# Optimization experiments

Measured on AMD Instinct MI355X. Metric: run time of the kernel, lower is better.

Reference implementation:

```python
import jax, jax.numpy as jnp
import numpy as np

B, L, C, H = 4, 1024, 768, 12
D = C // H  # head_ch = 64


def setup_inputs() -> dict:
    key = jax.random.key(0)
    ks = jax.random.split(key, 8)
    s = 1.0 / np.sqrt(C)
    return {
        "inputs_q": jax.random.normal(ks[0], (B, L, C), jnp.float32),
        "inputs_kv": jax.random.normal(ks[1], (B, L, C), jnp.float32),
        "Wq": jax.random.normal(ks[2], (C, H * D), jnp.float32) * s,
        "Wk": jax.random.normal(ks[3], (C, H * D), jnp.float32) * s,
        "Wv": jax.random.normal(ks[4], (C, H * D), jnp.float32) * s,
        "Wout": jax.random.normal(ks[5], (H * D, C), jnp.float32) * s,
        "W_pre": jax.random.normal(ks[6], (H, H), jnp.float32) * (1.0 / np.sqrt(H)),
        "W_post": jax.random.normal(ks[7], (H, H), jnp.float32) * (1.0 / np.sqrt(H)),
    }


def reference(inputs_q, inputs_kv, Wq, Wk, Wv, Wout, W_pre, W_post):
    # Linear projections (no bias), split into heads: b l (h d) -> b h l d
    def split_heads(x):
        b, l, _ = x.shape
        return x.reshape(b, l, H, D).transpose(0, 2, 1, 3)

    q = split_heads(inputs_q @ Wq) / jnp.sqrt(jnp.asarray(D, inputs_q.dtype))
    k = split_heads(inputs_kv @ Wk)
    v = split_heads(inputs_kv @ Wv)

    # Attention logits [b, h, l, k]
    weights = jnp.einsum('bhld,bhkd->bhlk', q, k)
    # Talking-heads: learned cross-head mixing pre-softmax
    weights = jnp.einsum('bhlk,hi->bilk', weights, W_pre)
    weights = jax.nn.softmax(weights, axis=-1)
    # Talking-heads post-softmax mixing
    weights = jnp.einsum('bhlk,hi->bilk', weights, W_post)

    scores = jnp.einsum('bhlk,bhkd->bhld', weights, v)
    scores = scores.transpose(0, 2, 1, 3).reshape(B, L, H * D)  # b l (h d)
    return scores @ Wout
```

## Files before the change

kernel.cpp:

```cpp
#include <hip/hip_runtime.h>

#define BB 4
#define LL 1024
#define CC 768
#define HH 12
#define DD 64

typedef unsigned short ushort_t;
typedef __attribute__((ext_vector_type(8))) short bf16x8;
typedef __attribute__((ext_vector_type(4))) float f32x4;

__device__ inline ushort_t f2bf(float x) {
    union { float f; unsigned u; } v; v.f = x;
    unsigned r = (v.u + 0x7FFFu + ((v.u >> 16) & 1u)) >> 16;
    return (ushort_t)r;
}
__device__ inline float bf2f(ushort_t u) {
    union { unsigned u; float f; } v; v.u = ((unsigned)u) << 16;
    return v.f;
}

__global__ __launch_bounds__(256) void cast_in(const float* __restrict__ q,
                                               const float* __restrict__ kv,
                                               ushort_t* __restrict__ qo,
                                               ushort_t* __restrict__ kvo) {
    const float* src = blockIdx.y ? kv : q;
    ushort_t* dst = blockIdx.y ? kvo : qo;
    size_t i = ((size_t)blockIdx.x * 256 + threadIdx.x) * 8;
    float4 a = *(const float4*)(src + i);
    float4 b = *(const float4*)(src + i + 4);
    ushort_t t[8] = {f2bf(a.x), f2bf(a.y), f2bf(a.z), f2bf(a.w),
                     f2bf(b.x), f2bf(b.y), f2bf(b.z), f2bf(b.w)};
    *(uint4*)(dst + i) = *(uint4*)t;
}

__global__ __launch_bounds__(256) void wt_cast(const float* __restrict__ w0, const float* __restrict__ w1,
                                               const float* __restrict__ w2, const float* __restrict__ w3,
                                               ushort_t* __restrict__ o0, ushort_t* __restrict__ o1,
                                               ushort_t* __restrict__ o2, ushort_t* __restrict__ o3) {
    const float* W = blockIdx.z == 0 ? w0 : blockIdx.z == 1 ? w1 : blockIdx.z == 2 ? w2 : w3;
    ushort_t* Wt   = blockIdx.z == 0 ? o0 : blockIdx.z == 1 ? o1 : blockIdx.z == 2 ? o2 : o3;
    __shared__ float t[32][33];
    const int c = threadIdx.x & 31, r0 = threadIdx.x >> 5;
    const int kb = blockIdx.x * 32, nb = blockIdx.y * 32;
#pragma unroll
    for (int i = 0; i < 4; ++i)
        t[r0 + 8 * i][c] = W[(size_t)(kb + r0 + 8 * i) * CC + nb + c];
    __syncthreads();
#pragma unroll
    for (int i = 0; i < 4; ++i)
        Wt[(size_t)(nb + r0 + 8 * i) * CC + kb + c] = f2bf(t[c][r0 + 8 * i]);
}

__global__ __launch_bounds__(256) void proj_gemm(const ushort_t* __restrict__ Aq,
                                                 const ushort_t* __restrict__ Akv,
                                                 const ushort_t* __restrict__ Wqt,
                                                 const ushort_t* __restrict__ Wkt,
                                                 const ushort_t* __restrict__ Wvt,
                                                 ushort_t* __restrict__ Qo,
                                                 ushort_t* __restrict__ Ko,
                                                 ushort_t* __restrict__ Vto) {
    const int z = blockIdx.z;
    const ushort_t* A  = (z == 0) ? Aq : Akv;
    const ushort_t* Wt = (z == 0) ? Wqt : (z == 1 ? Wkt : Wvt);

    __shared__ ushort_t a_lds[128 * 40];
    __shared__ ushort_t b_lds[128 * 40];

    const int tid = threadIdx.x;
    const int bm = blockIdx.x * 128, bn = blockIdx.y * 128;
    const int wave = tid >> 6, lane = tid & 63;
    const int quad = lane >> 4, lq = lane & 15;
    const int wr = wave >> 1, wc = wave & 1;

    f32x4 acc[4][4] = {};

    for (int k0 = 0; k0 < CC; k0 += 32) {
#pragma unroll
        for (int s = 0; s < 2; ++s) {
            int c = tid + s * 256;
            int row = c >> 2, ko = (c & 3) * 8;
            *(uint4*)&a_lds[row * 40 + ko] = *(const uint4*)&A[(size_t)(bm + row) * CC + k0 + ko];
            *(uint4*)&b_lds[row * 40 + ko] = *(const uint4*)&Wt[(size_t)(bn + row) * CC + k0 + ko];
        }
        __syncthreads();
        bf16x8 af[4], bfr[4];
#pragma unroll
        for (int mi = 0; mi < 4; ++mi)
            af[mi] = *(bf16x8*)&a_lds[(wr * 64 + mi * 16 + lq) * 40 + quad * 8];
#pragma unroll
        for (int ni = 0; ni < 4; ++ni)
            bfr[ni] = *(bf16x8*)&b_lds[(wc * 64 + ni * 16 + lq) * 40 + quad * 8];
#pragma unroll
        for (int mi = 0; mi < 4; ++mi)
#pragma unroll
            for (int ni = 0; ni < 4; ++ni)
                acc[mi][ni] = __builtin_amdgcn_mfma_f32_16x16x32_bf16(af[mi], bfr[ni], acc[mi][ni], 0, 0, 0);
        __syncthreads();
    }

    const float scale = (z == 0) ? 0.125f : 1.0f;
#pragma unroll
    for (int mi = 0; mi < 4; ++mi)
#pragma unroll
        for (int ni = 0; ni < 4; ++ni)
#pragma unroll
            for (int r = 0; r < 4; ++r) {
                int row = bm + wr * 64 + mi * 16 + quad * 4 + r;
                int col = bn + wc * 64 + ni * 16 + lq;
                int b = row >> 10, l = row & 1023, h = col >> 6, d = col & 63;
                ushort_t v = f2bf(acc[mi][ni][r] * scale);
                if (z == 0)      Qo[((size_t)(b * HH + h) * LL + l) * DD + d] = v;
                else if (z == 1) Ko[((size_t)(b * HH + h) * LL + l) * DD + d] = v;
                else             Vto[((size_t)(b * HH + h) * DD + d) * LL + l] = v;
            }
}

__global__ __launch_bounds__(256) void qk_gemm(const ushort_t* __restrict__ Q,
                                               const ushort_t* __restrict__ K,
                                               ushort_t* __restrict__ S) {
    __shared__ ushort_t a_lds[128 * 40];
    __shared__ ushort_t b_lds[128 * 40];

    const int tid = threadIdx.x;
    const int bm = blockIdx.x * 128, bn = blockIdx.y * 128;
    const int bh = blockIdx.z;
    const ushort_t* Qh = Q + (size_t)bh * LL * DD;
    const ushort_t* Kh = K + (size_t)bh * LL * DD;
    const int wave = tid >> 6, lane = tid & 63;
    const int quad = lane >> 4, lq = lane & 15;
    const int wr = wave >> 1, wc = wave & 1;

    f32x4 acc[4][4] = {};

    for (int k0 = 0; k0 < DD; k0 += 32) {
#pragma unroll
        for (int s = 0; s < 2; ++s) {
            int c = tid + s * 256;
            int row = c >> 2, ko = (c & 3) * 8;
            *(uint4*)&a_lds[row * 40 + ko] = *(const uint4*)&Qh[(size_t)(bm + row) * DD + k0 + ko];
            *(uint4*)&b_lds[row * 40 + ko] = *(const uint4*)&Kh[(size_t)(bn + row) * DD + k0 + ko];
        }
        __syncthreads();
        bf16x8 af[4], bfr[4];
#pragma unroll
        for (int mi = 0; mi < 4; ++mi)
            af[mi] = *(bf16x8*)&a_lds[(wr * 64 + mi * 16 + lq) * 40 + quad * 8];
#pragma unroll
        for (int ni = 0; ni < 4; ++ni)
            bfr[ni] = *(bf16x8*)&b_lds[(wc * 64 + ni * 16 + lq) * 40 + quad * 8];
#pragma unroll
        for (int mi = 0; mi < 4; ++mi)
#pragma unroll
            for (int ni = 0; ni < 4; ++ni)
                acc[mi][ni] = __builtin_amdgcn_mfma_f32_16x16x32_bf16(af[mi], bfr[ni], acc[mi][ni], 0, 0, 0);
        __syncthreads();
    }

#pragma unroll
    for (int mi = 0; mi < 4; ++mi)
#pragma unroll
        for (int ni = 0; ni < 4; ++ni)
#pragma unroll
            for (int r = 0; r < 4; ++r) {
                int row = bm + wr * 64 + mi * 16 + quad * 4 + r;
                int col = bn + wc * 64 + ni * 16 + lq;
                S[((size_t)bh * LL + row) * LL + col] = f2bf(acc[mi][ni][r]);
            }
}

__global__ __launch_bounds__(256) void mix_softmax(ushort_t* __restrict__ S,
                                                   const float* __restrict__ Wpre,
                                                   const float* __restrict__ Wpost) {
    __shared__ float s[HH][LL];
    __shared__ float wpre[HH][HH];
    __shared__ float wpost[HH][HH];

    const int tid = threadIdx.x;
    const int l = blockIdx.x;
    const int b = blockIdx.y;

    if (tid < HH * HH) {
        wpre[tid / HH][tid % HH] = Wpre[tid];
        wpost[tid / HH][tid % HH] = Wpost[tid];
    }

    for (int idx = tid; idx < HH * 128; idx += 256) {
        int h = idx >> 7, c = idx & 127;
        uint4 raw = *(const uint4*)&S[((size_t)(b * HH + h) * LL + l) * LL + c * 8];
        ushort_t* u = (ushort_t*)&raw;
#pragma unroll
        for (int j = 0; j < 8; ++j) s[h][c * 8 + j] = bf2f(u[j]);
    }
    __syncthreads();

    for (int k = tid; k < LL; k += 256) {
        float sv[HH], mx[HH];
#pragma unroll
        for (int h = 0; h < HH; ++h) sv[h] = s[h][k];
#pragma unroll
        for (int i = 0; i < HH; ++i) {
            float a = 0.f;
#pragma unroll
            for (int h = 0; h < HH; ++h) a += sv[h] * wpre[h][i];
            mx[i] = a;
        }
#pragma unroll
        for (int i = 0; i < HH; ++i) s[i][k] = mx[i];
    }
    __syncthreads();

    {
        const int wave = tid >> 6;
        const int lane = tid & 63;
        for (int h = wave; h < HH; h += 4) {
            float vals[16];
            float m = -1e30f;
#pragma unroll
            for (int j = 0; j < 16; ++j) {
                vals[j] = s[h][lane + 64 * j];
                m = fmaxf(m, vals[j]);
            }
#pragma unroll
            for (int off = 32; off; off >>= 1) m = fmaxf(m, __shfl_xor(m, off));
            float sum = 0.f;
#pragma unroll
            for (int j = 0; j < 16; ++j) {
                vals[j] = __expf(vals[j] - m);
                sum += vals[j];
            }
#pragma unroll
            for (int off = 32; off; off >>= 1) sum += __shfl_xor(sum, off);
            float inv = 1.0f / sum;
#pragma unroll
            for (int j = 0; j < 16; ++j) s[h][lane + 64 * j] = vals[j] * inv;
        }
    }
    __syncthreads();

    for (int k = tid; k < LL; k += 256) {
        float sv[HH], mx[HH];
#pragma unroll
        for (int h = 0; h < HH; ++h) sv[h] = s[h][k];
#pragma unroll
        for (int i = 0; i < HH; ++i) {
            float a = 0.f;
#pragma unroll
            for (int h = 0; h < HH; ++h) a += sv[h] * wpost[h][i];
            mx[i] = a;
        }
#pragma unroll
        for (int i = 0; i < HH; ++i) s[i][k] = mx[i];
    }
    __syncthreads();

    for (int idx = tid; idx < HH * 128; idx += 256) {
        int h = idx >> 7, c = idx & 127;
        ushort_t u[8];
#pragma unroll
        for (int j = 0; j < 8; ++j) u[j] = f2bf(s[h][c * 8 + j]);
        *(uint4*)&S[((size_t)(b * HH + h) * LL + l) * LL + c * 8] = *(uint4*)u;
    }
}

__global__ __launch_bounds__(256) void pv_gemm(const ushort_t* __restrict__ P,
                                               const ushort_t* __restrict__ Vt,
                                               ushort_t* __restrict__ att) {
    __shared__ ushort_t a_lds[128 * 40];
    __shared__ ushort_t b_lds[64 * 40];

    const int tid = threadIdx.x;
    const int bm = blockIdx.x * 128;
    const int bh = blockIdx.y;
    const int b = bh / HH, ih = bh % HH;
    const ushort_t* Ph = P + ((size_t)bh << 20);
    const ushort_t* Vh = Vt + (size_t)bh * LL * DD;
    const int wave = tid >> 6, lane = tid & 63;
    const int quad = lane >> 4, lq = lane & 15;
    const int wr = wave >> 1, wc = wave & 1;

    f32x4 acc[4][2] = {};

    for (int k0 = 0; k0 < LL; k0 += 32) {
#pragma unroll
        for (int s = 0; s < 2; ++s) {
            int c = tid + s * 256;
            int row = c >> 2, ko = (c & 3) * 8;
            *(uint4*)&a_lds[row * 40 + ko] = *(const uint4*)&Ph[(size_t)(bm + row) * LL + k0 + ko];
        }
        {
            int row = tid >> 2, ko = (tid & 3) * 8;
            *(uint4*)&b_lds[row * 40 + ko] = *(const uint4*)&Vh[(size_t)row * LL + k0 + ko];
        }
        __syncthreads();
        bf16x8 af[4], bfr[2];
#pragma unroll
        for (int mi = 0; mi < 4; ++mi)
            af[mi] = *(bf16x8*)&a_lds[(wr * 64 + mi * 16 + lq) * 40 + quad * 8];
#pragma unroll
        for (int ni = 0; ni < 2; ++ni)
            bfr[ni] = *(bf16x8*)&b_lds[(wc * 32 + ni * 16 + lq) * 40 + quad * 8];
#pragma unroll
        for (int mi = 0; mi < 4; ++mi)
#pragma unroll
            for (int ni = 0; ni < 2; ++ni)
                acc[mi][ni] = __builtin_amdgcn_mfma_f32_16x16x32_bf16(af[mi], bfr[ni], acc[mi][ni], 0, 0, 0);
        __syncthreads();
    }

#pragma unroll
    for (int mi = 0; mi < 4; ++mi)
#pragma unroll
        for (int ni = 0; ni < 2; ++ni)
#pragma unroll
            for (int r = 0; r < 4; ++r) {
                int lrow = bm + wr * 64 + mi * 16 + quad * 4 + r;
                int col = wc * 32 + ni * 16 + lq;
                att[((size_t)(b * LL) + lrow) * CC + ih * DD + col] = f2bf(acc[mi][ni][r]);
            }
}

__global__ __launch_bounds__(256) void out_gemm(const ushort_t* __restrict__ A,
                                                const ushort_t* __restrict__ Wt,
                                                float* __restrict__ out) {
    __shared__ ushort_t a_lds[128 * 40];
    __shared__ ushort_t b_lds[128 * 40];

    const int tid = threadIdx.x;
    const int bm = blockIdx.x * 128, bn = blockIdx.y * 128;
    const int wave = tid >> 6, lane = tid & 63;
    const int quad = lane >> 4, lq = lane & 15;
    const int wr = wave >> 1, wc = wave & 1;

    f32x4 acc[4][4] = {};

    for (int k0 = 0; k0 < CC; k0 += 32) {
#pragma unroll
        for (int s = 0; s < 2; ++s) {
            int c = tid + s * 256;
            int row = c >> 2, ko = (c & 3) * 8;
            *(uint4*)&a_lds[row * 40 + ko] = *(const uint4*)&A[(size_t)(bm + row) * CC + k0 + ko];
            *(uint4*)&b_lds[row * 40 + ko] = *(const uint4*)&Wt[(size_t)(bn + row) * CC + k0 + ko];
        }
        __syncthreads();
        bf16x8 af[4], bfr[4];
#pragma unroll
        for (int mi = 0; mi < 4; ++mi)
            af[mi] = *(bf16x8*)&a_lds[(wr * 64 + mi * 16 + lq) * 40 + quad * 8];
#pragma unroll
        for (int ni = 0; ni < 4; ++ni)
            bfr[ni] = *(bf16x8*)&b_lds[(wc * 64 + ni * 16 + lq) * 40 + quad * 8];
#pragma unroll
        for (int mi = 0; mi < 4; ++mi)
#pragma unroll
            for (int ni = 0; ni < 4; ++ni)
                acc[mi][ni] = __builtin_amdgcn_mfma_f32_16x16x32_bf16(af[mi], bfr[ni], acc[mi][ni], 0, 0, 0);
        __syncthreads();
    }

#pragma unroll
    for (int mi = 0; mi < 4; ++mi)
#pragma unroll
        for (int ni = 0; ni < 4; ++ni)
#pragma unroll
            for (int r = 0; r < 4; ++r) {
                int row = bm + wr * 64 + mi * 16 + quad * 4 + r;
                int col = bn + wc * 64 + ni * 16 + lq;
                out[(size_t)row * CC + col] = acc[mi][ni][r];
            }
}

extern "C" void kernel_launch(void* const* d_in, const int* in_sizes, int n_in,
                              void* d_out, int out_size, void* d_ws, size_t ws_size,
                              hipStream_t stream) {
    const float* inputs_q  = (const float*)d_in[0];
    const float* inputs_kv = (const float*)d_in[1];
    const float* Wq   = (const float*)d_in[2];
    const float* Wk   = (const float*)d_in[3];
    const float* Wv   = (const float*)d_in[4];
    const float* Wout = (const float*)d_in[5];
    const float* Wpre  = (const float*)d_in[6];
    const float* Wpost = (const float*)d_in[7];
    float* out = (float*)d_out;

    const size_t nS   = (size_t)BB * HH * LL * LL;
    const size_t nQKV = (size_t)BB * HH * LL * DD;
    const size_t nW   = (size_t)CC * CC;

    ushort_t* Sb   = (ushort_t*)d_ws;
    ushort_t* Qb   = Sb + nS;
    ushort_t* Kb   = Qb + nQKV;
    ushort_t* Vtb  = Kb + nQKV;
    ushort_t* attb = Vtb + nQKV;
    ushort_t* inq  = attb + nQKV;
    ushort_t* inkv = inq + nQKV;
    ushort_t* Wqt  = inkv + nQKV;
    ushort_t* Wkt  = Wqt + nW;
    ushort_t* Wvt  = Wkt + nW;
    ushort_t* Wot  = Wvt + nW;

    dim3 blk(256);

    cast_in<<<dim3(1536, 2), blk, 0, stream>>>(inputs_q, inputs_kv, inq, inkv);
    wt_cast<<<dim3(24, 24, 4), blk, 0, stream>>>(Wq, Wk, Wv, Wout, Wqt, Wkt, Wvt, Wot);
    proj_gemm<<<dim3(32, 6, 3), blk, 0, stream>>>(inq, inkv, Wqt, Wkt, Wvt, Qb, Kb, Vtb);
    qk_gemm<<<dim3(8, 8, BB * HH), blk, 0, stream>>>(Qb, Kb, Sb);
    mix_softmax<<<dim3(LL, BB), blk, 0, stream>>>(Sb, Wpre, Wpost);
    pv_gemm<<<dim3(8, BB * HH), blk, 0, stream>>>(Sb, Vtb, attb);
    out_gemm<<<dim3(32, 6), blk, 0, stream>>>(attb, Wot, out);
}
```

Measured before the change: 269.7 us.

## Stage GEMM tiles via global_load_lds, halve pv tile, vectorize softmax LDS staging

Replaces register-staged global-to-LDS tile copies in all four GEMM kernels with direct global_load_lds 16-byte transfers into unpadded 32-element-wide LDS rows. The pv_gemm tile shrinks from 128 to 64 rows, doubling its grid, and mix_softmax switches to 4-wide loads and float4 LDS writes. The aim is to cut VGPR traffic and instruction count on the load path and raise pv_gemm occupancy. Dropping the row padding may cause LDS bank conflicts on the fragment reads.

```diff
diff --git a/kernel.cpp b/kernel.cpp
--- a/kernel.cpp
+++ b/kernel.cpp
@@ -18,6 +18,19 @@
 __device__ inline float bf2f(ushort_t u) {
     union { unsigned u; float f; } v; v.u = ((unsigned)u) << 16;
     return v.f;
+}
+
+__device__ inline void stage_rows(const ushort_t* __restrict__ g, int stride,
+                                  ushort_t* lds, int nbytes, int wave, int lane) {
+    const int ko = (lane & 3) << 3;
+    const int rsub = lane >> 2;
+    for (int off = wave * 1024; off < nbytes; off += 4096) {
+        int row = (off >> 6) + rsub;
+        __builtin_amdgcn_global_load_lds(
+            (const __attribute__((address_space(1))) void*)(g + (size_t)row * stride + ko),
+            (__attribute__((address_space(3))) void*)(lds + (off >> 1)),
+            16, 0, 0);
+    }
 }
 
 __global__ __launch_bounds__(256) void cast_in(const float* __restrict__ q,
@@ -64,8 +77,8 @@
     const ushort_t* A  = (z == 0) ? Aq : Akv;
     const ushort_t* Wt = (z == 0) ? Wqt : (z == 1 ? Wkt : Wvt);
 
-    __shared__ ushort_t a_lds[128 * 40];
-    __shared__ ushort_t b_lds[128 * 40];
+    __shared__ __align__(16) ushort_t a_lds[128 * 32];
+    __shared__ __align__(16) ushort_t b_lds[128 * 32];
 
     const int tid = threadIdx.x;
     const int bm = blockIdx.x * 128, bn = blockIdx.y * 128;
@@ -76,21 +89,16 @@
     f32x4 acc[4][4] = {};
 
     for (int k0 = 0; k0 < CC; k0 += 32) {
-#pragma unroll
-        for (int s = 0; s < 2; ++s) {
-            int c = tid + s * 256;
-            int row = c >> 2, ko = (c & 3) * 8;
-            *(uint4*)&a_lds[row * 40 + ko] = *(const uint4*)&A[(size_t)(bm + row) * CC + k0 + ko];
-            *(uint4*)&b_lds[row * 40 + ko] = *(const uint4*)&Wt[(size_t)(bn + row) * CC + k0 + ko];
-        }
+        stage_rows(A + (size_t)bm * CC + k0, CC, a_lds, 8192, wave, lane);
+        stage_rows(Wt + (size_t)bn * CC + k0, CC, b_lds, 8192, wave, lane);
         __syncthreads();
         bf16x8 af[4], bfr[4];
 #pragma unroll
         for (int mi = 0; mi < 4; ++mi)
-            af[mi] = *(bf16x8*)&a_lds[(wr * 64 + mi * 16 + lq) * 40 + quad * 8];
-#pragma unroll
-        for (int ni = 0; ni < 4; ++ni)
-            bfr[ni] = *(bf16x8*)&b_lds[(wc * 64 + ni * 16 + lq) * 40 + quad * 8];
+            af[mi] = *(bf16x8*)&a_lds[(wr * 64 + mi * 16 + lq) * 32 + quad * 8];
+#pragma unroll
+        for (int ni = 0; ni < 4; ++ni)
+            bfr[ni] = *(bf16x8*)&b_lds[(wc * 64 + ni * 16 + lq) * 32 + quad * 8];
 #pragma unroll
         for (int mi = 0; mi < 4; ++mi)
 #pragma unroll
@@ -119,8 +127,8 @@
 __global__ __launch_bounds__(256) void qk_gemm(const ushort_t* __restrict__ Q,
                                                const ushort_t* __restrict__ K,
                                                ushort_t* __restrict__ S) {
-    __shared__ ushort_t a_lds[128 * 40];
-    __shared__ ushort_t b_lds[128 * 40];
+    __shared__ __align__(16) ushort_t a_lds[128 * 32];
+    __shared__ __align__(16) ushort_t b_lds[128 * 32];
 
     const int tid = threadIdx.x;
     const int bm = blockIdx.x * 128, bn = blockIdx.y * 128;
@@ -134,21 +142,16 @@
     f32x4 acc[4][4] = {};
 
     for (int k0 = 0; k0 < DD; k0 += 32) {
-#pragma unroll
-        for (int s = 0; s < 2; ++s) {
-            int c = tid + s * 256;
-            int row = c >> 2, ko = (c & 3) * 8;
-            *(uint4*)&a_lds[row * 40 + ko] = *(const uint4*)&Qh[(size_t)(bm + row) * DD + k0 + ko];
-            *(uint4*)&b_lds[row * 40 + ko] = *(const uint4*)&Kh[(size_t)(bn + row) * DD + k0 + ko];
-        }
+        stage_rows(Qh + (size_t)bm * DD + k0, DD, a_lds, 8192, wave, lane);
+        stage_rows(Kh + (size_t)bn * DD + k0, DD, b_lds, 8192, wave, lane);
         __syncthreads();
         bf16x8 af[4], bfr[4];
 #pragma unroll
         for (int mi = 0; mi < 4; ++mi)
-            af[mi] = *(bf16x8*)&a_lds[(wr * 64 + mi * 16 + lq) * 40 + quad * 8];
-#pragma unroll
-        for (int ni = 0; ni < 4; ++ni)
-            bfr[ni] = *(bf16x8*)&b_lds[(wc * 64 + ni * 16 + lq) * 40 + quad * 8];
+            af[mi] = *(bf16x8*)&a_lds[(wr * 64 + mi * 16 + lq) * 32 + quad * 8];
+#pragma unroll
+        for (int ni = 0; ni < 4; ++ni)
+            bfr[ni] = *(bf16x8*)&b_lds[(wc * 64 + ni * 16 + lq) * 32 + quad * 8];
 #pragma unroll
         for (int mi = 0; mi < 4; ++mi)
 #pragma unroll
@@ -185,12 +188,12 @@
         wpost[tid / HH][tid % HH] = Wpost[tid];
     }
 
-    for (int idx = tid; idx < HH * 128; idx += 256) {
-        int h = idx >> 7, c = idx & 127;
-        uint4 raw = *(const uint4*)&S[((size_t)(b * HH + h) * LL + l) * LL + c * 8];
+    for (int idx = tid; idx < HH * 256; idx += 256) {
+        int h = idx >> 8, c = idx & 255;
+        uint2 raw = *(const uint2*)&S[((size_t)(b * HH + h) * LL + l) * LL + c * 4];
         ushort_t* u = (ushort_t*)&raw;
-#pragma unroll
-        for (int j = 0; j < 8; ++j) s[h][c * 8 + j] = bf2f(u[j]);
+        float4 f = make_float4(bf2f(u[0]), bf2f(u[1]), bf2f(u[2]), bf2f(u[3]));
+        ((float4*)s[h])[c] = f;
     }
     __syncthreads();
 
@@ -254,23 +257,22 @@
     }
     __syncthreads();
 
-    for (int idx = tid; idx < HH * 128; idx += 256) {
-        int h = idx >> 7, c = idx & 127;
-        ushort_t u[8];
-#pragma unroll
-        for (int j = 0; j < 8; ++j) u[j] = f2bf(s[h][c * 8 + j]);
-        *(uint4*)&S[((size_t)(b * HH + h) * LL + l) * LL + c * 8] = *(uint4*)u;
+    for (int idx = tid; idx < HH * 256; idx += 256) {
+        int h = idx >> 8, c = idx & 255;
+        float4 f = ((float4*)s[h])[c];
+        ushort_t u[4] = {f2bf(f.x), f2bf(f.y), f2bf(f.z), f2bf(f.w)};
+        *(uint2*)&S[((size_t)(b * HH + h) * LL + l) * LL + c * 4] = *(uint2*)u;
     }
 }
 
 __global__ __launch_bounds__(256) void pv_gemm(const ushort_t* __restrict__ P,
                                                const ushort_t* __restrict__ Vt,
                                                ushort_t* __restrict__ att) {
-    __shared__ ushort_t a_lds[128 * 40];
-    __shared__ ushort_t b_lds[64 * 40];
+    __shared__ __align__(16) ushort_t a_lds[64 * 32];
+    __shared__ __align__(16) ushort_t b_lds[64 * 32];
 
     const int tid = threadIdx.x;
-    const int bm = blockIdx.x * 128;
+    const int bm = blockIdx.x * 64;
     const int bh = blockIdx.y;
     const int b = bh / HH, ih = bh % HH;
     const ushort_t* Ph = P + ((size_t)bh << 20);
@@ -279,29 +281,21 @@
     const int quad = lane >> 4, lq = lane & 15;
     const int wr = wave >> 1, wc = wave & 1;
 
-    f32x4 acc[4][2] = {};
+    f32x4 acc[2][2] = {};
 
     for (int k0 = 0; k0 < LL; k0 += 32) {
-#pragma unroll
-        for (int s = 0; s < 2; ++s) {
-            int c = tid + s * 256;
-            int row = c >> 2, ko = (c & 3) * 8;
-            *(uint4*)&a_lds[row * 40 + ko] = *(const uint4*)&Ph[(size_t)(bm + row) * LL + k0 + ko];
-        }
-        {
-            int row = tid >> 2, ko = (tid & 3) * 8;
-            *(uint4*)&b_lds[row * 40 + ko] = *(const uint4*)&Vh[(size_t)row * LL + k0 + ko];
-        }
-        __syncthreads();
-        bf16x8 af[4], bfr[2];
-#pragma unroll
-        for (int mi = 0; mi < 4; ++mi)
-            af[mi] = *(bf16x8*)&a_lds[(wr * 64 + mi * 16 + lq) * 40 + quad * 8];
+        stage_rows(Ph + (size_t)bm * LL + k0, LL, a_lds, 4096, wave, lane);
+        stage_rows(Vh + k0, LL, b_lds, 4096, wave, lane);
+        __syncthreads();
+        bf16x8 af[2], bfr[2];
+#pragma unroll
+        for (int mi = 0; mi < 2; ++mi)
+            af[mi] = *(bf16x8*)&a_lds[(wr * 32 + mi * 16 + lq) * 32 + quad * 8];
 #pragma unroll
         for (int ni = 0; ni < 2; ++ni)
-            bfr[ni] = *(bf16x8*)&b_lds[(wc * 32 + ni * 16 + lq) * 40 + quad * 8];
-#pragma unroll
-        for (int mi = 0; mi < 4; ++mi)
+            bfr[ni] = *(bf16x8*)&b_lds[(wc * 32 + ni * 16 + lq) * 32 + quad * 8];
+#pragma unroll
+        for (int mi = 0; mi < 2; ++mi)
 #pragma unroll
             for (int ni = 0; ni < 2; ++ni)
                 acc[mi][ni] = __builtin_amdgcn_mfma_f32_16x16x32_bf16(af[mi], bfr[ni], acc[mi][ni], 0, 0, 0);
@@ -309,12 +303,12 @@
     }
 
 #pragma unroll
-    for (int mi = 0; mi < 4; ++mi)
+    for (int mi = 0; mi < 2; ++mi)
 #pragma unroll
         for (int ni = 0; ni < 2; ++ni)
 #pragma unroll
             for (int r = 0; r < 4; ++r) {
-                int lrow = bm + wr * 64 + mi * 16 + quad * 4 + r;
+                int lrow = bm + wr * 32 + mi * 16 + quad * 4 + r;
                 int col = wc * 32 + ni * 16 + lq;
                 att[((size_t)(b * LL) + lrow) * CC + ih * DD + col] = f2bf(acc[mi][ni][r]);
             }
@@ -323,8 +317,8 @@
 __global__ __launch_bounds__(256) void out_gemm(const ushort_t* __restrict__ A,
                                                 const ushort_t* __restrict__ Wt,
                                                 float* __restrict__ out) {
-    __shared__ ushort_t a_lds[128 * 40];
-    __shared__ ushort_t b_lds[128 * 40];
+    __shared__ __align__(16) ushort_t a_lds[128 * 32];
+    __shared__ __align__(16) ushort_t b_lds[128 * 32];
 
     const int tid = threadIdx.x;
     const int bm = blockIdx.x * 128, bn = blockIdx.y * 128;
@@ -335,21 +329,16 @@
     f32x4 acc[4][4] = {};
 
     for (int k0 = 0; k0 < CC; k0 += 32) {
-#pragma unroll
-        for (int s = 0; s < 2; ++s) {
-            int c = tid + s * 256;
-            int row = c >> 2, ko = (c & 3) * 8;
-            *(uint4*)&a_lds[row * 40 + ko] = *(const uint4*)&A[(size_t)(bm + row) * CC + k0 + ko];
-            *(uint4*)&b_lds[row * 40 + ko] = *(const uint4*)&Wt[(size_t)(bn + row) * CC + k0 + ko];
-        }
+        stage_rows(A + (size_t)bm * CC + k0, CC, a_lds, 8192, wave, lane);
+        stage_rows(Wt + (size_t)bn * CC + k0, CC, b_lds, 8192, wave, lane);
         __syncthreads();
         bf16x8 af[4], bfr[4];
 #pragma unroll
         for (int mi = 0; mi < 4; ++mi)
-            af[mi] = *(bf16x8*)&a_lds[(wr * 64 + mi * 16 + lq) * 40 + quad * 8];
-#pragma unroll
-        for (int ni = 0; ni < 4; ++ni)
-            bfr[ni] = *(bf16x8*)&b_lds[(wc * 64 + ni * 16 + lq) * 40 + quad * 8];
+            af[mi] = *(bf16x8*)&a_lds[(wr * 64 + mi * 16 + lq) * 32 + quad * 8];
+#pragma unroll
+        for (int ni = 0; ni < 4; ++ni)
+            bfr[ni] = *(bf16x8*)&b_lds[(wc * 64 + ni * 16 + lq) * 32 + quad * 8];
 #pragma unroll
         for (int mi = 0; mi < 4; ++mi)
 #pragma unroll
@@ -406,6 +395,6 @@
     proj_gemm<<<dim3(32, 6, 3), blk, 0, stream>>>(inq, inkv, Wqt, Wkt, Wvt, Qb, Kb, Vtb);
     qk_gemm<<<dim3(8, 8, BB * HH), blk, 0, stream>>>(Qb, Kb, Sb);
     mix_softmax<<<dim3(LL, BB), blk, 0, stream>>>(Sb, Wpre, Wpost);
-    pv_gemm<<<dim3(8, BB * HH), blk, 0, stream>>>(Sb, Vtb, attb);
+    pv_gemm<<<dim3(16, BB * HH), blk, 0, stream>>>(Sb, Vtb, attb);
     out_gemm<<<dim3(32, 6), blk, 0, stream>>>(attb, Wot, out);
 }
```

New measurement: 272.4 us. No clear change (+1.0%).
